# Kernel tuning notes

Measured on AMD Instinct MI355X. Metric: run time of the kernel, lower is better.

## Reference

```python
import jax, jax.numpy as jnp
import numpy as np

KS = 3  # deformable kernel size

def conv2d(x, w, pad, stride=1):
    return jax.lax.conv_general_dilated(
        x, w, (stride, stride), [(pad, pad), (pad, pad)],
        dimension_numbers=('NCHW', 'OIHW', 'NCHW'))

def deform_conv(x, wp, bp, wc):
    # Faithful port of DeformConv2d(inc, outc, kernel_size=3, padding=1, stride=1)
    b, c, h, w = x.shape
    N = KS * KS
    offset = conv2d(x, wp, 1) + bp[None, :, None, None]  # [b, 2N, h, w]
    xpad = jnp.pad(x, ((0, 0), (0, 0), (1, 1), (1, 1)))
    Hp, Wp = h + 2, w + 2
    # p_n: kernel-relative offsets (x coords first, then y coords)
    rng = jnp.arange(-(KS - 1) // 2, (KS - 1) // 2 + 1, dtype=x.dtype)
    pnx, pny = jnp.meshgrid(rng, rng, indexing='ij')
    p_n = jnp.concatenate([pnx.reshape(-1), pny.reshape(-1)])  # [2N]
    # p_0: base sampling grid (1-indexed into padded map)
    p0x = jnp.broadcast_to(jnp.arange(1, h + 1, dtype=x.dtype)[:, None], (h, w))
    p0y = jnp.broadcast_to(jnp.arange(1, w + 1, dtype=x.dtype)[None, :], (h, w))
    p0 = jnp.concatenate([jnp.broadcast_to(p0x, (N, h, w)),
                          jnp.broadcast_to(p0y, (N, h, w))], 0)  # [2N,h,w]
    p = p0[None] + p_n[None, :, None, None] + offset  # [b,2N,h,w]
    p = jnp.transpose(p, (0, 2, 3, 1))  # [b,h,w,2N]
    qf = jax.lax.stop_gradient(jnp.floor(p))
    qltx = jnp.clip(qf[..., :N], 0, Hp - 1)
    qlty = jnp.clip(qf[..., N:], 0, Wp - 1)
    qrbx = jnp.clip(qf[..., :N] + 1, 0, Hp - 1)
    qrby = jnp.clip(qf[..., N:] + 1, 0, Wp - 1)
    px = jnp.clip(p[..., :N], 0, Hp - 1)
    py = jnp.clip(p[..., N:], 0, Wp - 1)
    g_lt = (1 + (qltx - px)) * (1 + (qlty - py))
    g_rb = (1 - (qrbx - px)) * (1 - (qrby - py))
    g_lb = (1 + (qltx - px)) * (1 - (qrby - py))
    g_rt = (1 - (qrbx - px)) * (1 + (qlty - py))
    xflat = xpad.reshape(b, c, Hp * Wp)
    def gather(qx, qy):
        idx = (qx.astype(jnp.int32) * Wp + qy.astype(jnp.int32)).reshape(b, 1, -1)
        idx = jnp.broadcast_to(idx, (b, c, idx.shape[-1]))
        return jnp.take_along_axis(xflat, idx, axis=2).reshape(b, c, h, w, N)
    xo = (g_lt[:, None] * gather(qltx, qlty) + g_rb[:, None] * gather(qrbx, qrby)
          + g_lb[:, None] * gather(qltx, qrby) + g_rt[:, None] * gather(qrbx, qlty))
    # rearrange 'b c h w (i j) -> b c (h i) (w j)'
    xo = xo.reshape(b, c, h, w, KS, KS).transpose(0, 1, 2, 4, 3, 5).reshape(b, c, h * KS, w * KS)
    return conv2d(xo, wc, 1, stride=KS)


def setup_inputs() -> dict:
    key = jax.random.key(0)
    B, C, H, W = 4, 64, 256, 256
    DIM, S0 = 64, 5
    ks = jax.random.split(key, 14)
    s = 0.02
    inp = {
        'x': jax.random.normal(ks[0], (B, C, H, W), jnp.float32),
        'wp_a': jax.random.normal(ks[1], (2 * KS * KS, C, 3, 3), jnp.float32) * s,
        'bp_a': jnp.zeros((2 * KS * KS,), jnp.float32),
        'wc_a': jax.random.normal(ks[2], (C, C, KS, KS), jnp.float32) * s,
        'w1_a': jax.random.normal(ks[3], (C, C, 1, 1), jnp.float32) * s,
        'b1_a': jax.random.normal(ks[4], (C,), jnp.float32) * s,
        'wp_p': jax.random.normal(ks[5], (2 * KS * KS, C, 3, 3), jnp.float32) * s,
        'bp_p': jnp.zeros((2 * KS * KS,), jnp.float32),
        'wc_p': jax.random.normal(ks[6], (C, C, KS, KS), jnp.float32) * s,
        'w1_p': jax.random.normal(ks[7], (C, C, 1, 1), jnp.float32) * s,
        'b1_p': jax.random.normal(ks[8], (C,), jnp.float32) * s,
        'w0': jax.random.normal(ks[9], (DIM, C, S0, S0), jnp.float32) * s,
        'b0': jax.random.normal(ks[10], (DIM,), jnp.float32) * s,
    }
    return inp


def reference(x, wp_a, bp_a, wc_a, w1_a, b1_a, wp_p, bp_p, wc_p, w1_p, b1_p, w0, b0):
    H, W = x.shape[2], x.shape[3]
    xf = jnp.fft.rfft2(x, axes=(2, 3))
    amp = jnp.abs(xf)
    pha = jnp.angle(xf)
    amp3 = deform_conv(amp, wp_a, bp_a, wc_a)
    amp1 = conv2d(amp, w1_a, 0) + b1_a[None, :, None, None]
    pha3 = deform_conv(pha, wp_p, bp_p, wc_p)
    pha1 = conv2d(pha, w1_p, 0) + b1_p[None, :, None, None]
    eps = 1e-08
    real_13 = amp1 * jnp.cos(pha3) + eps
    imag_31 = amp3 * jnp.sin(pha1) + eps
    real_31 = amp3 * jnp.cos(pha1) + eps
    imag_13 = amp1 * jnp.sin(pha3) + eps
    out_c = (real_13 + real_31) + 1j * (imag_31 + imag_13) + eps
    xr = jnp.abs(jnp.fft.irfft2(out_c, s=(H, W), axes=(2, 3)))
    s0 = w0.shape[2]
    return conv2d(xr, w0, s0 // 2) + b0[None, :, None, None]
```

## Files before the change

kernel.cpp:

```cpp
#include <hip/hip_runtime.h>
#include <math.h>

#define BB 4
#define CC 64
#define HH 256
#define WW 256
#define WF 129
#define NPIX (WF*HH)
#define NS ((size_t)BB*CC*NPIX)
#define TWOPI 6.283185307179586f

typedef __attribute__((ext_vector_type(8))) short short8v;
typedef __attribute__((ext_vector_type(4))) float float4v;

__device__ __forceinline__ float2 cmulf(float2 a, float2 b) {
    return make_float2(a.x*b.x - a.y*b.y, a.x*b.y + a.y*b.x);
}

template<int SIGN>
__device__ __forceinline__ float2 fft256_lds(const float2* __restrict__ xs,
                                             float2* __restrict__ ys,
                                             const float2* __restrict__ tw,
                                             const float2* __restrict__ tw16,
                                             int t) {
    int k1 = t & 15, n2 = t >> 4;
    float2 acc = make_float2(0.f, 0.f);
    #pragma unroll
    for (int n1 = 0; n1 < 16; ++n1) {
        float2 v = xs[n1*16 + n2];
        float2 w = tw16[(n1*k1) & 15];
        float ws = (SIGN < 0) ? -w.y : w.y;
        acc.x = fmaf(v.x, w.x, fmaf(-v.y, ws, acc.x));
        acc.y = fmaf(v.x, ws, fmaf( v.y, w.x, acc.y));
    }
    float2 w2 = tw[n2*k1];
    float w2s = (SIGN < 0) ? -w2.y : w2.y;
    ys[t] = cmulf(acc, make_float2(w2.x, w2s));
    __syncthreads();
    float2 acc2 = make_float2(0.f, 0.f);
    #pragma unroll
    for (int m2 = 0; m2 < 16; ++m2) {
        float2 v = ys[m2*16 + k1];
        float2 w = tw16[(m2*n2) & 15];
        float ws = (SIGN < 0) ? -w.y : w.y;
        acc2.x = fmaf(v.x, w.x, fmaf(-v.y, ws, acc2.x));
        acc2.y = fmaf(v.x, ws, fmaf( v.y, w.x, acc2.y));
    }
    return acc2;
}

template<int SIGN>
__device__ __forceinline__ float2 fft256_ip(float2* __restrict__ buf,
                                            const float2* __restrict__ tw,
                                            const float2* __restrict__ tw16,
                                            int t) {
    int k1 = t & 15, n2 = t >> 4;
    float2 acc = make_float2(0.f, 0.f);
    #pragma unroll
    for (int n1 = 0; n1 < 16; ++n1) {
        float2 v = buf[n1*16 + n2];
        float2 w = tw16[(n1*k1) & 15];
        float ws = (SIGN < 0) ? -w.y : w.y;
        acc.x = fmaf(v.x, w.x, fmaf(-v.y, ws, acc.x));
        acc.y = fmaf(v.x, ws, fmaf( v.y, w.x, acc.y));
    }
    float2 w2 = tw[n2*k1];
    float w2s = (SIGN < 0) ? -w2.y : w2.y;
    float2 mid = cmulf(acc, make_float2(w2.x, w2s));
    __syncthreads();
    buf[t] = mid;
    __syncthreads();
    float2 acc2 = make_float2(0.f, 0.f);
    #pragma unroll
    for (int m2 = 0; m2 < 16; ++m2) {
        float2 v = buf[m2*16 + k1];
        float2 w = tw16[(m2*n2) & 15];
        float ws = (SIGN < 0) ? -w.y : w.y;
        acc2.x = fmaf(v.x, w.x, fmaf(-v.y, ws, acc2.x));
        acc2.y = fmaf(v.x, ws, fmaf( v.y, w.x, acc2.y));
    }
    return acc2;
}

__global__ void k_tw(float2* __restrict__ twg) {
    int m = threadIdx.x;
    float s, c;
    sincosf((TWOPI/256.f) * (float)m, &s, &c);
    twg[m] = make_float2(c, s);
}

__global__ __launch_bounds__(256) void k_fft_rows(const float* __restrict__ x,
                                                  const float2* __restrict__ twg,
                                                  float* __restrict__ r1re,
                                                  float* __restrict__ r1im) {
    __shared__ float2 work[256];
    __shared__ float tileRe[16][132], tileIm[16][132];
    __shared__ float2 tw[256];
    __shared__ float2 tw16[16];
    int t = threadIdx.x;
    int bid = blockIdx.x;
    int yt = bid & 15;
    int bc = bid >> 4;
    int y0 = yt*16;
    tw[t] = twg[t];
    if (t < 16) tw16[t] = twg[t*16];
    const float* xb = x + (size_t)bc*HH*WW + (size_t)y0*WW;
    for (int r = 0; r < 16; ++r) {
        __syncthreads();
        work[t] = make_float2(xb[r*WW + t], 0.f);
        __syncthreads();
        float2 X = fft256_ip<-1>(work, tw, tw16, t);
        if (t < WF) { tileRe[r][t] = X.x; tileIm[r][t] = X.y; }
    }
    __syncthreads();
    if (t < WF) {
        size_t base = ((size_t)bc*WF + t)*HH + y0;
        #pragma unroll
        for (int g = 0; g < 4; ++g) {
            float4 vr = make_float4(tileRe[g*4][t], tileRe[g*4+1][t],
                                    tileRe[g*4+2][t], tileRe[g*4+3][t]);
            float4 vi = make_float4(tileIm[g*4][t], tileIm[g*4+1][t],
                                    tileIm[g*4+2][t], tileIm[g*4+3][t]);
            *(float4*)&r1re[base + g*4] = vr;
            *(float4*)&r1im[base + g*4] = vi;
        }
    }
}

__global__ __launch_bounds__(256) void k_fft_cols(const float* __restrict__ r1re,
                                                  const float* __restrict__ r1im,
                                                  const float2* __restrict__ twg,
                                                  float* __restrict__ amp,
                                                  float* __restrict__ pha) {
    __shared__ float2 xs[256], ys[256];
    __shared__ float2 tw[256];
    __shared__ float2 tw16[16];
    int t = threadIdx.x;
    int bid = blockIdx.x;
    int k = bid % WF;
    int bc = bid / WF;
    size_t base = ((size_t)bc*WF + k)*HH;
    tw[t] = twg[t];
    if (t < 16) tw16[t] = twg[t*16];
    xs[t] = make_float2(r1re[base + t], r1im[base + t]);
    __syncthreads();
    float2 X = fft256_lds<-1>(xs, ys, tw, tw16, t);
    amp[base + t] = sqrtf(X.x*X.x + X.y*X.y);
    pha[base + t] = atan2f(X.y, X.x);
}

__global__ __launch_bounds__(256) void k_pack(const float* __restrict__ src,
                                              float* __restrict__ dst) {
    __shared__ float tile[64][65];
    int tid = threadIdx.x;
    int bid = blockIdx.x;
    int it = bid & 3;
    int rest = bid >> 2;
    int k = rest % WF;
    int b = rest / WF;
    int i0 = it*64;
    int ii = tid & 63;
    int cg = tid >> 6;
    for (int rep = 0; rep < 16; ++rep) {
        int c = cg*16 + rep;
        tile[c][ii] = src[(size_t)(b*CC + c)*NPIX + (size_t)k*HH + i0 + ii];
    }
    __syncthreads();
    for (int rep = 0; rep < 16; ++rep) {
        int m = cg*16 + rep;
        dst[((size_t)(b*WF + k)*HH + i0 + m)*CC + ii] = tile[ii][m];
    }
}

__device__ __forceinline__ unsigned short bf16r(float f) {
    unsigned u = __float_as_uint(f);
    unsigned r = (u + 0x7FFFu + ((u >> 16) & 1u)) >> 16;
    return (unsigned short)r;
}
__device__ __forceinline__ float bf16f(unsigned short h) {
    return __uint_as_float(((unsigned)h) << 16);
}

__global__ void k_wct(const float* __restrict__ wc,
                      unsigned short* __restrict__ wh,
                      unsigned short* __restrict__ wl) {
    int idx = blockIdx.x*256 + threadIdx.x;
    if (idx < 64*576) {
        int k = idx % 576;
        int oc = idx / 576;
        int pos = k >> 6;
        int c = k & 63;
        float v = wc[((size_t)oc*64 + c)*9 + pos];
        unsigned short h = bf16r(v);
        wh[idx] = h;
        wl[idx] = bf16r(v - bf16f(h));
    }
}

__global__ void k_wsplit(const float* __restrict__ w0,
                         unsigned short* __restrict__ whT,
                         unsigned short* __restrict__ wlT) {
    int idx = blockIdx.x*256 + threadIdx.x;
    if (idx < 25*64*64) {
        int c = idx & 63;
        int t = idx >> 6;
        int oc = t & 63;
        int tap = t >> 6;
        float v = w0[((size_t)oc*CC + c)*25 + tap];
        unsigned short h = bf16r(v);
        float l = v - bf16f(h);
        whT[idx] = h;
        wlT[idx] = bf16r(l);
    }
}

__global__ void k_wpt(const float* __restrict__ wpa, const float* __restrict__ wpp,
                      float* __restrict__ wta, float* __restrict__ wtp) {
    int idx = blockIdx.x*256 + threadIdx.x;
    if (idx < 64*162) {
        int c = idx / 162;
        int r = idx - c*162;
        int oc = r / 9, pos = r - oc*9;
        size_t s = ((size_t)oc*CC + c)*9 + pos;
        wta[idx] = wpa[s];
        wtp[idx] = wpp[s];
    }
}

__global__ __launch_bounds__(256) void k_off2(const float* __restrict__ amp,
                                              const float* __restrict__ pha,
                                              const float* __restrict__ wptA,
                                              const float* __restrict__ wptP,
                                              const float* __restrict__ bpA,
                                              const float* __restrict__ bpP,
                                              float* __restrict__ offa,
                                              float* __restrict__ offp) {
    __shared__ float colb[2][3][260];
    int tid = threadIdx.x;
    int bid = blockIdx.x;
    int sel = (bid >= BB*WF) ? 1 : 0;
    int rb = sel ? bid - BB*WF : bid;
    int j = rb % WF;
    int b = rb / WF;
    const float* img = sel ? pha : amp;
    const float* wpt = sel ? wptP : wptA;
    const float* bp  = sel ? bpP  : bpA;
    float* off = sel ? offp : offa;

    const float* ib = img + (size_t)b*CC*NPIX + (size_t)j*HH;
    bool jm = (j > 0), jp = (j < WF-1);

    float acc[18];
    #pragma unroll
    for (int o = 0; o < 18; ++o) acc[o] = bp[o];

    if (tid < 12) {
        int bufi = tid & 1;
        int dj = (tid >> 1) % 3;
        int e = tid / 6;
        colb[bufi][dj][e ? 257 : 0] = 0.f;
    }
    {
        const float* cb = ib;
        colb[0][1][tid+1] = cb[tid];
        colb[0][0][tid+1] = jm ? cb[tid - HH] : 0.f;
        colb[0][2][tid+1] = jp ? cb[tid + HH] : 0.f;
    }
    __syncthreads();

    for (int c = 0; c < CC; ++c) {
        int cur = c & 1;
        if (c + 1 < CC) {
            const float* cb = ib + (size_t)(c+1)*NPIX;
            colb[cur^1][1][tid+1] = cb[tid];
            colb[cur^1][0][tid+1] = jm ? cb[tid - HH] : 0.f;
            colb[cur^1][2][tid+1] = jp ? cb[tid + HH] : 0.f;
        }
        float v[9];
        #pragma unroll
        for (int di = 0; di < 3; ++di)
            #pragma unroll
            for (int dj = 0; dj < 3; ++dj)
                v[di*3+dj] = colb[cur][dj][tid + di];
        const float* wc = wpt + c*162;
        #pragma unroll
        for (int o = 0; o < 18; ++o) {
            #pragma unroll
            for (int p = 0; p < 9; ++p)
                acc[o] = fmaf(wc[o*9+p], v[p], acc[o]);
        }
        __syncthreads();
    }

    size_t ob = ((size_t)(b*18)*WF + j)*HH + tid;
    #pragma unroll
    for (int o = 0; o < 18; ++o)
        off[ob + (size_t)o*WF*HH] = acc[o];
}

#define SPAD 328
__global__ __launch_bounds__(256) void k_deform(const float* __restrict__ imgc,
                                                const float* __restrict__ off,
                                                const unsigned short* __restrict__ wh,
                                                const unsigned short* __restrict__ wl,
                                                float* __restrict__ out) {
    __shared__ int   cidx[4][144];
    __shared__ float cwgt[4][144];
    __shared__ __align__(16) unsigned short Sh[16][SPAD];
    __shared__ __align__(16) unsigned short Sl[16][SPAD];
    int tid = threadIdx.x;
    int bid = blockIdx.x;
    int it = bid & 15;
    int rest = bid >> 4;
    int j = rest % WF;
    int b = rest / WF;
    int i0 = it * 16;

    if (tid < 144) {
        int pix = tid / 9;
        int pos = tid % 9;
        int ki = pos / 3, kj = pos % 3;
        int i = i0 + pix;
        int r = 3*i + ki - 1;
        int s = 3*j + kj - 1;
        float g[4] = {0.f,0.f,0.f,0.f};
        int ix[4] = {-1,-1,-1,-1};
        if (r >= 0 && s >= 0) {
            int hq = r/3, nx = r%3;
            int wq = s/3, ny = s%3;
            int n = nx*3 + ny;
            float ox = off[((size_t)(b*18 + n)*WF + wq)*HH + hq];
            float oy = off[((size_t)(b*18 + 9 + n)*WF + wq)*HH + hq];
            float pxf = (float)(hq + nx) + ox;
            float pyf = (float)(wq + ny) + oy;
            float qx = floorf(pxf), qy = floorf(pyf);
            float qltx = fminf(fmaxf(qx, 0.f), 257.f);
            float qlty = fminf(fmaxf(qy, 0.f), 130.f);
            float qrbx = fminf(fmaxf(qx + 1.f, 0.f), 257.f);
            float qrby = fminf(fmaxf(qy + 1.f, 0.f), 130.f);
            float pxc = fminf(fmaxf(pxf, 0.f), 257.f);
            float pyc = fminf(fmaxf(pyf, 0.f), 130.f);
            float glt = (1.f + (qltx - pxc)) * (1.f + (qlty - pyc));
            float grb = (1.f - (qrbx - pxc)) * (1.f - (qrby - pyc));
            float glb = (1.f + (qltx - pxc)) * (1.f - (qrby - pyc));
            float grt = (1.f - (qrbx - pxc)) * (1.f + (qlty - pyc));
            int ax0 = (int)qltx, ax1 = (int)qrbx;
            int ay0 = (int)qlty, ay1 = (int)qrby;
            int cx[4] = {ax0, ax1, ax0, ax1};
            int cy[4] = {ay0, ay1, ay1, ay0};
            g[0]=glt; g[1]=grb; g[2]=glb; g[3]=grt;
            #pragma unroll
            for (int q = 0; q < 4; ++q) {
                int a = cx[q], bq = cy[q];
                ix[q] = (a >= 1 && a <= 256 && bq >= 1 && bq <= 129)
                        ? ((bq-1)*HH + (a-1))*CC : -1;
            }
        }
        #pragma unroll
        for (int q = 0; q < 4; ++q) { cidx[q][tid] = ix[q]; cwgt[q][tid] = g[q]; }
    }
    __syncthreads();

    const float* cb = imgc + (size_t)b * (size_t)WF * HH * CC;
    int lane = tid & 63;
    int w = tid >> 6;
    int l15 = lane & 15;
    int l4 = lane >> 4;
    float4v acc = {0.f, 0.f, 0.f, 0.f};
    const unsigned short* wbh = wh + (size_t)(w*16 + l15)*576 + l4*8;
    const unsigned short* wbl = wl + (size_t)(w*16 + l15)*576 + l4*8;

    for (int t = tid; t < 4096; t += 256) {
        int c = t & 63;
        int s = t >> 6;
        int pix = s >> 2, pos = s & 3;
        int combo = pix*9 + pos;
        float sum = 0.f;
        #pragma unroll
        for (int q = 0; q < 4; ++q) {
            int ofs = cidx[q][combo];
            float v = (ofs >= 0) ? cb[(size_t)ofs + c] : 0.f;
            sum += cwgt[q][combo] * v;
        }
        unsigned short h = bf16r(sum);
        Sh[pix][pos*64 + c] = h;
        Sl[pix][pos*64 + c] = bf16r(sum - bf16f(h));
    }
    __syncthreads();
    #pragma unroll
    for (int k0 = 0; k0 < 256; k0 += 32) {
        short8v Ah = *(const short8v*)&wbh[k0];
        short8v Al = *(const short8v*)&wbl[k0];
        short8v Bh = *(const short8v*)&Sh[l15][k0 + l4*8];
        short8v Bl = *(const short8v*)&Sl[l15][k0 + l4*8];
        acc = __builtin_amdgcn_mfma_f32_16x16x32_bf16(Ah, Bh, acc, 0, 0, 0);
        acc = __builtin_amdgcn_mfma_f32_16x16x32_bf16(Ah, Bl, acc, 0, 0, 0);
        acc = __builtin_amdgcn_mfma_f32_16x16x32_bf16(Al, Bh, acc, 0, 0, 0);
    }
    __syncthreads();

    for (int t = tid; t < 5120; t += 256) {
        int c = t & 63;
        int s = t >> 6;
        int pix = s / 5, pp = s - pix*5;
        int combo = pix*9 + 4 + pp;
        float sum = 0.f;
        #pragma unroll
        for (int q = 0; q < 4; ++q) {
            int ofs = cidx[q][combo];
            float v = (ofs >= 0) ? cb[(size_t)ofs + c] : 0.f;
            sum += cwgt[q][combo] * v;
        }
        unsigned short h = bf16r(sum);
        Sh[pix][pp*64 + c] = h;
        Sl[pix][pp*64 + c] = bf16r(sum - bf16f(h));
    }
    __syncthreads();
    #pragma unroll
    for (int k0 = 0; k0 < 320; k0 += 32) {
        short8v Ah = *(const short8v*)&wbh[256 + k0];
        short8v Al = *(const short8v*)&wbl[256 + k0];
        short8v Bh = *(const short8v*)&Sh[l15][k0 + l4*8];
        short8v Bl = *(const short8v*)&Sl[l15][k0 + l4*8];
        acc = __builtin_amdgcn_mfma_f32_16x16x32_bf16(Ah, Bh, acc, 0, 0, 0);
        acc = __builtin_amdgcn_mfma_f32_16x16x32_bf16(Ah, Bl, acc, 0, 0, 0);
        acc = __builtin_amdgcn_mfma_f32_16x16x32_bf16(Al, Bh, acc, 0, 0, 0);
    }

    size_t ob = (size_t)b*CC*NPIX + (size_t)j*HH + i0;
    #pragma unroll
    for (int r = 0; r < 4; ++r) {
        int oc = w*16 + l4*4 + r;
        out[ob + (size_t)oc*NPIX + l15] = acc[r];
    }
}

__global__ __launch_bounds__(256) void k_combine(const float* __restrict__ ampc,
                                                 const float* __restrict__ phac,
                                                 float* __restrict__ a3,
                                                 float* __restrict__ p3,
                                                 const float* __restrict__ w1a,
                                                 const float* __restrict__ b1a,
                                                 const float* __restrict__ w1p,
                                                 const float* __restrict__ b1p) {
    __shared__ float la[64][65], lp[64][65];
    int tid = threadIdx.x;
    int bid = blockIdx.x;
    int quarter = bid & 3;
    int rest = bid >> 2;
    int j = rest % WF;
    int b = rest / WF;
    int i0 = quarter * 64;
    size_t gbase = ((size_t)(b*WF + j)*HH + i0) * CC;
    for (int rep = 0; rep < 16; ++rep) {
        int t = rep*256 + tid;
        int pix = t >> 6;
        int c = t & 63;
        la[c][pix] = ampc[gbase + t];
        lp[c][pix] = phac[gbase + t];
    }
    __syncthreads();
    int ii = tid & 63;
    int wv = tid >> 6;
    float acc_a[16], acc_p[16];
    #pragma unroll
    for (int q = 0; q < 16; ++q) { acc_a[q] = b1a[wv*16+q]; acc_p[q] = b1p[wv*16+q]; }
    for (int c = 0; c < CC; ++c) {
        float av = la[c][ii], pv = lp[c][ii];
        #pragma unroll
        for (int q = 0; q < 16; ++q) {
            acc_a[q] += w1a[(wv*16+q)*CC + c] * av;
            acc_p[q] += w1p[(wv*16+q)*CC + c] * pv;
        }
    }
    #pragma unroll
    for (int q = 0; q < 16; ++q) {
        int oc = wv*16 + q;
        size_t idx = (size_t)(b*CC + oc)*NPIX + (size_t)j*HH + i0 + ii;
        float a3v = a3[idx];
        float p3v = p3[idx];
        float s1, c1, s3, c3;
        sincosf(acc_p[q], &s1, &c1);
        sincosf(p3v, &s3, &c3);
        float re = acc_a[q]*c3 + a3v*c1 + 3e-8f;
        float im = a3v*s1 + acc_a[q]*s3 + 2e-8f;
        a3[idx] = re;
        p3[idx] = im;
    }
}

__global__ __launch_bounds__(256) void k_ifft_cols(const float* __restrict__ ocre,
                                                   const float* __restrict__ ocim,
                                                   const float2* __restrict__ twg,
                                                   float* __restrict__ r2re,
                                                   float* __restrict__ r2im) {
    __shared__ float2 xs[256], ys[256];
    __shared__ float2 tw[256];
    __shared__ float2 tw16[16];
    int t = threadIdx.x;
    int bid = blockIdx.x;
    int k = bid % WF;
    int bc = bid / WF;
    size_t base = ((size_t)bc*WF + k)*HH;
    tw[t] = twg[t];
    if (t < 16) tw16[t] = twg[t*16];
    xs[t] = make_float2(ocre[base + t], ocim[base + t]);
    __syncthreads();
    float2 X = fft256_lds<1>(xs, ys, tw, tw16, t);
    r2re[base + t] = X.x * (1.0f/256.0f);
    r2im[base + t] = X.y * (1.0f/256.0f);
}

__global__ __launch_bounds__(256) void k_irfft_rows(const float* __restrict__ r2re,
                                                    const float* __restrict__ r2im,
                                                    const float2* __restrict__ twg,
                                                    float* __restrict__ xr) {
    __shared__ float2 work[256];
    __shared__ float tileRe[16][132], tileIm[16][132];
    __shared__ float2 tw[256];
    __shared__ float2 tw16[16];
    int t = threadIdx.x;
    int bid = blockIdx.x;
    int yt = bid & 15;
    int bc = bid >> 4;
    int y0 = yt*16;
    tw[t] = twg[t];
    if (t < 16) tw16[t] = twg[t*16];
    if (t < WF) {
        size_t base = ((size_t)bc*WF + t)*HH + y0;
        #pragma unroll
        for (int g = 0; g < 4; ++g) {
            float4 vr = *(const float4*)&r2re[base + g*4];
            float4 vi = *(const float4*)&r2im[base + g*4];
            tileRe[g*4+0][t] = vr.x; tileIm[g*4+0][t] = vi.x;
            tileRe[g*4+1][t] = vr.y; tileIm[g*4+1][t] = vi.y;
            tileRe[g*4+2][t] = vr.z; tileIm[g*4+2][t] = vi.z;
            tileRe[g*4+3][t] = vr.w; tileIm[g*4+3][t] = vi.w;
        }
    }
    __syncthreads();
    float* xb = xr + (size_t)bc*HH*WW + (size_t)y0*WW;
    int src = (t < WF) ? t : 256 - t;
    float sg = (t < WF) ? 1.f : -1.f;
    for (int r = 0; r < 16; ++r) {
        work[t] = make_float2(tileRe[r][src], sg*tileIm[r][src]);
        __syncthreads();
        float2 X = fft256_ip<1>(work, tw, tw16, t);
        xb[r*WW + t] = fabsf(X.x * (1.0f/256.0f));
        __syncthreads();
    }
}

__global__ __launch_bounds__(256) void k_split(const float* __restrict__ xr,
                                               unsigned short* __restrict__ xh,
                                               unsigned short* __restrict__ xl) {
    __shared__ float tile[64][65];
    int tid = threadIdx.x;
    int bid = blockIdx.x;
    int q = bid & 3;
    int y = (bid >> 2) & 255;
    int b = bid >> 10;
    int x0 = q*64;
    int lane = tid & 63;
    int cg = tid >> 6;
    for (int rep = 0; rep < 16; ++rep) {
        int c = cg*16 + rep;
        tile[c][lane] = xr[(((size_t)(b*CC + c)*HH + y)*WW) + x0 + lane];
    }
    __syncthreads();
    int x = tid >> 2;
    int c0 = (tid & 3)*8;
    #pragma unroll
    for (int ch = 0; ch < 2; ++ch) {
        short8v hv, lv;
        #pragma unroll
        for (int j = 0; j < 8; ++j) {
            float v = tile[ch*32 + c0 + j][x];
            unsigned short h = bf16r(v);
            float l = v - bf16f(h);
            hv[j] = (short)h;
            lv[j] = (short)bf16r(l);
        }
        size_t ob = ((((size_t)(b*2 + ch)*HH + y)*WW) + x0 + x)*32 + c0;
        *(short8v*)&xh[ob] = hv;
        *(short8v*)&xl[ob] = lv;
    }
}

#define LROW 40
#define LX 72
#define LROWS 6
#define PLANE (LROWS*LX*LROW)
#define NSLOT 7

__global__ __launch_bounds__(256) void k_conv5m(const unsigned short* __restrict__ xh,
                                                const unsigned short* __restrict__ xl,
                                                const unsigned short* __restrict__ whT,
                                                const unsigned short* __restrict__ wlT,
                                                const float* __restrict__ b0,
                                                float* __restrict__ out) {
    __shared__ unsigned short smem[2*PLANE];
    int tid = threadIdx.x;
    int bid = blockIdx.x;
    int q = bid & 3;
    int yb = (bid >> 2) & 127;
    int b = bid >> 9;
    int x0 = q*64;
    int y0 = yb*2;
    int lane = tid & 63;
    int w = tid >> 6;
    int wrow = w >> 1;
    int oc0 = (w & 1)*32;
    int l15 = lane & 15;
    int l4  = lane >> 4;

    int goff[NSLOT], loff[NSLOT];
    bool inb[NSLOT], okimg[NSLOT];
    #pragma unroll
    for (int s = 0; s < NSLOT; ++s) {
        int it = tid + s*256;
        int part = it & 3;
        int idx = it >> 2;
        int row = idx / LX;
        int xi = idx - row*LX;
        int gy = y0 + row - 2;
        int gx = x0 + xi - 2;
        bool ib = (it < LROWS*LX*4);
        bool ok = ib && gy >= 0 && gy < HH && gx >= 0 && gx < WW;
        inb[s] = ib;
        okimg[s] = ok;
        goff[s] = ok ? ((gy*WW + gx)*32 + part*8) : 0;
        loff[s] = ib ? ((row*LX + xi)*LROW + part*8) : 0;
    }

    float4v acc[2][4];
    #pragma unroll
    for (int o = 0; o < 2; ++o) {
        float4v bi;
        #pragma unroll
        for (int r = 0; r < 4; ++r) bi[r] = b0[oc0 + o*16 + l4*4 + r];
        #pragma unroll
        for (int p = 0; p < 4; ++p) acc[o][p] = bi;
    }

    short8v rh[NSLOT], rl[NSLOT];
    const short8v zero8 = {0,0,0,0,0,0,0,0};

#define PREFETCH(CH) do { \
        size_t chb = ((size_t)(b*2 + (CH)) << 16) * 32; \
        _Pragma("unroll") \
        for (int s = 0; s < NSLOT; ++s) { \
            rh[s] = *(const short8v*)&xh[chb + goff[s]]; \
            rl[s] = *(const short8v*)&xl[chb + goff[s]]; \
        } \
    } while (0)

#define WRITE() do { \
        _Pragma("unroll") \
        for (int s = 0; s < NSLOT; ++s) { \
            if (inb[s]) { \
                *(short8v*)&smem[loff[s]]         = okimg[s] ? rh[s] : zero8; \
                *(short8v*)&smem[PLANE + loff[s]] = okimg[s] ? rl[s] : zero8; \
            } \
        } \
    } while (0)

#define LOADA(TAP, CH, A0, A1, A2, A3r) do { \
        size_t wb = ((size_t)(TAP)*64 + oc0 + l15)*64 + (size_t)(CH)*32 + l4*8; \
        A0  = *(const short8v*)&whT[wb]; \
        A1  = *(const short8v*)&whT[wb + 1024]; \
        A2  = *(const short8v*)&wlT[wb]; \
        A3r = *(const short8v*)&wlT[wb + 1024]; \
    } while (0)

#define LOADB(TAP, B_h, B_l) do { \
        int dy = (TAP)/5, dx = (TAP) - dy*5; \
        int rbase = (wrow + dy)*LX + l15 + dx; \
        _Pragma("unroll") \
        for (int p = 0; p < 4; ++p) { \
            int a = (rbase + p*16)*LROW + l4*8; \
            B_h[p] = *(const short8v*)&smem[a]; \
            B_l[p] = *(const short8v*)&smem[a + PLANE]; \
        } \
    } while (0)

#define MFMAS(A0, A1, A2, A3r, B_h, B_l) do { \
        _Pragma("unroll") for (int p = 0; p < 4; ++p) \
            acc[0][p] = __builtin_amdgcn_mfma_f32_16x16x32_bf16(A0, B_h[p], acc[0][p], 0, 0, 0); \
        _Pragma("unroll") for (int p = 0; p < 4; ++p) \
            acc[1][p] = __builtin_amdgcn_mfma_f32_16x16x32_bf16(A1, B_h[p], acc[1][p], 0, 0, 0); \
        _Pragma("unroll") for (int p = 0; p < 4; ++p) \
            acc[0][p] = __builtin_amdgcn_mfma_f32_16x16x32_bf16(A0, B_l[p], acc[0][p], 0, 0, 0); \
        _Pragma("unroll") for (int p = 0; p < 4; ++p) \
            acc[1][p] = __builtin_amdgcn_mfma_f32_16x16x32_bf16(A1, B_l[p], acc[1][p], 0, 0, 0); \
        _Pragma("unroll") for (int p = 0; p < 4; ++p) \
            acc[0][p] = __builtin_amdgcn_mfma_f32_16x16x32_bf16(A2, B_h[p], acc[0][p], 0, 0, 0); \
        _Pragma("unroll") for (int p = 0; p < 4; ++p) \
            acc[1][p] = __builtin_amdgcn_mfma_f32_16x16x32_bf16(A3r, B_h[p], acc[1][p], 0, 0, 0); \
    } while (0)

#define COMPUTE(CH) do { \
        short8v cA0, cA1, cA2, cA3, nA0, nA1, nA2, nA3; \
        short8v cBh[4], cBl[4]; \
        LOADA(0, CH, cA0, cA1, cA2, cA3); \
        _Pragma("unroll 5") \
        for (int tap = 0; tap < 25; ++tap) { \
            if (tap < 24) LOADA(tap+1, CH, nA0, nA1, nA2, nA3); \
            LOADB(tap, cBh, cBl); \
            MFMAS(cA0, cA1, cA2, cA3, cBh, cBl); \
            if (tap < 24) { cA0 = nA0; cA1 = nA1; cA2 = nA2; cA3 = nA3; } \
        } \
    } while (0)

    PREFETCH(0);
    WRITE();
    __syncthreads();
    PREFETCH(1);
    COMPUTE(0);
    __syncthreads();
    WRITE();
    __syncthreads();
    COMPUTE(1);

#undef PREFETCH
#undef WRITE
#undef LOADA
#undef LOADB
#undef MFMAS
#undef COMPUTE

    int y = y0 + wrow;
    #pragma unroll
    for (int o = 0; o < 2; ++o) {
        #pragma unroll
        for (int p = 0; p < 4; ++p) {
            #pragma unroll
            for (int r = 0; r < 4; ++r) {
                int oc = oc0 + o*16 + l4*4 + r;
                int x = x0 + p*16 + l15;
                out[(((size_t)(b*CC + oc)*HH + y)*WW) + x] = acc[o][p][r];
            }
        }
    }
}

extern "C" void kernel_launch(void* const* d_in, const int* in_sizes, int n_in,
                              void* d_out, int out_size, void* d_ws, size_t ws_size,
                              hipStream_t stream) {
    const float* x    = (const float*)d_in[0];
    const float* wp_a = (const float*)d_in[1];
    const float* bp_a = (const float*)d_in[2];
    const float* wc_a = (const float*)d_in[3];
    const float* w1_a = (const float*)d_in[4];
    const float* b1_a = (const float*)d_in[5];
    const float* wp_p = (const float*)d_in[6];
    const float* bp_p = (const float*)d_in[7];
    const float* wc_p = (const float*)d_in[8];
    const float* w1_p = (const float*)d_in[9];
    const float* b1_p = (const float*)d_in[10];
    const float* w0   = (const float*)d_in[11];
    const float* b0   = (const float*)d_in[12];
    float* out = (float*)d_out;
    float* ws  = (float*)d_ws;

    float* R0 = ws;
    float* R1 = ws + 2*NS;
    float* R2 = ws + 4*NS;

    float* r1re = R0;
    float* r1im = R0 + NS;
    float* amp  = R1;
    float* pha  = R1 + NS;
    float* ampc = R0;
    float* phac = R0 + NS;
    size_t offsz = (size_t)BB*18*NPIX;
    float* offa = R2;
    float* offp = R2 + offsz;
    unsigned short* wsp = (unsigned short*)(R2 + 2*offsz);
    unsigned short* whA = wsp;
    unsigned short* wlA = wsp + 36864;
    unsigned short* whP = wsp + 2*36864;
    unsigned short* wlP = wsp + 3*36864;
    unsigned short* whT = wsp + 4*36864;
    unsigned short* wlT = whT + 25*64*64;
    float* wptA = (float*)(wlT + 25*64*64);
    float* wptP = wptA + 64*162;
    float2* twg = (float2*)(wptP + 64*162);
    float* A3   = R1;
    float* P3   = R1 + NS;
    float* r2re = R0;
    float* r2im = R0 + NS;
    float* xrp  = R1;
    unsigned short* xhp = (unsigned short*)R0;
    unsigned short* xlp = xhp + (size_t)BB*2*HH*WW*32;

    k_tw<<<1, 256, 0, stream>>>(twg);
    k_wct<<<144, 256, 0, stream>>>(wc_a, whA, wlA);
    k_wct<<<144, 256, 0, stream>>>(wc_p, whP, wlP);
    k_wsplit<<<400, 256, 0, stream>>>(w0, whT, wlT);
    k_wpt<<<41, 256, 0, stream>>>(wp_a, wp_p, wptA, wptP);
    k_fft_rows<<<BB*CC*16, 256, 0, stream>>>(x, twg, r1re, r1im);
    k_fft_cols<<<BB*CC*WF, 256, 0, stream>>>(r1re, r1im, twg, amp, pha);
    k_pack<<<BB*WF*4, 256, 0, stream>>>(amp, ampc);
    k_pack<<<BB*WF*4, 256, 0, stream>>>(pha, phac);
    k_off2<<<2*BB*WF, 256, 0, stream>>>(amp, pha, wptA, wptP, bp_a, bp_p, offa, offp);
    k_deform<<<BB*WF*16, 256, 0, stream>>>(ampc, offa, whA, wlA, A3);
    k_deform<<<BB*WF*16, 256, 0, stream>>>(phac, offp, whP, wlP, P3);
    k_combine<<<BB*WF*4, 256, 0, stream>>>(ampc, phac, A3, P3, w1_a, b1_a, w1_p, b1_p);
    k_ifft_cols<<<BB*CC*WF, 256, 0, stream>>>(A3, P3, twg, r2re, r2im);
    k_irfft_rows<<<BB*CC*16, 256, 0, stream>>>(r2re, r2im, twg, xrp);
    k_split<<<BB*HH*4, 256, 0, stream>>>(xrp, xhp, xlp);
    k_conv5m<<<BB*128*4, 256, 0, stream>>>(xhp, xlp, whT, wlT, b0, out);
}
```

Measured before the change: 1.454 ms.

## Rework final 5x5 conv to 32x32x16 MFMA with 4-row tiles

The final 5x5 convolution kernel moves from 16x16x32 bf16 MFMAs to 32x32x16 MFMAs. Each block now covers 4 output rows (one per wave) and all 64 output channels, so the grid is halved. The input channel dimension is staged through LDS in four 16-channel phases with register prefetch, which shrinks the LDS tile and adds more syncs. The aim is fewer LDS B-operand reads per MFMA flop and better weight reuse, at the cost of dropping the A-operand prefetch and adding sync points.

```diff
diff --git a/kernel.cpp b/kernel.cpp
--- a/kernel.cpp
+++ b/kernel.cpp
@@ -12,6 +12,7 @@
 
 typedef __attribute__((ext_vector_type(8))) short short8v;
 typedef __attribute__((ext_vector_type(4))) float float4v;
+typedef __attribute__((ext_vector_type(16))) float float16v;
 
 __device__ __forceinline__ float2 cmulf(float2 a, float2 b) {
     return make_float2(a.x*b.x - a.y*b.y, a.x*b.y + a.y*b.x);
@@ -587,11 +588,9 @@
     }
 }
 
-#define LROW 40
-#define LX 72
-#define LROWS 6
-#define PLANE (LROWS*LX*LROW)
-#define NSLOT 7
+#define CLX 68
+#define CPART 544
+#define CPLANE 1088
 
 __global__ __launch_bounds__(256) void k_conv5m(const unsigned short* __restrict__ xh,
                                                 const unsigned short* __restrict__ xl,
@@ -599,116 +598,99 @@
                                                 const unsigned short* __restrict__ wlT,
                                                 const float* __restrict__ b0,
                                                 float* __restrict__ out) {
-    __shared__ unsigned short smem[2*PLANE];
+    __shared__ __align__(16) unsigned short smem[2*CPLANE*8];
     int tid = threadIdx.x;
     int bid = blockIdx.x;
     int q = bid & 3;
-    int yb = (bid >> 2) & 127;
-    int b = bid >> 9;
+    int yb = (bid >> 2) & 63;
+    int b = bid >> 8;
     int x0 = q*64;
-    int y0 = yb*2;
+    int y0 = yb*4;
     int lane = tid & 63;
     int w = tid >> 6;
-    int wrow = w >> 1;
-    int oc0 = (w & 1)*32;
-    int l15 = lane & 15;
-    int l4  = lane >> 4;
-
-    int goff[NSLOT], loff[NSLOT];
-    bool inb[NSLOT], okimg[NSLOT];
-    #pragma unroll
-    for (int s = 0; s < NSLOT; ++s) {
-        int it = tid + s*256;
-        int part = it & 3;
-        int idx = it >> 2;
-        int row = idx / LX;
-        int xi = idx - row*LX;
+    int l31 = lane & 31;
+    int l1  = lane >> 5;
+
+    int goffb[5], loffs[5];
+    bool ok[5], has[5];
+    #pragma unroll
+    for (int s = 0; s < 5; ++s) {
+        int item = (s < 4) ? (s*256 + tid) : (1024 + tid);
+        bool h = (s < 4) || (tid < 64);
+        int part = (item >= CPART) ? 1 : 0;
+        int rest = item - part*CPART;
+        int row = rest / CLX;
+        int xi = rest - row*CLX;
         int gy = y0 + row - 2;
         int gx = x0 + xi - 2;
-        bool ib = (it < LROWS*LX*4);
-        bool ok = ib && gy >= 0 && gy < HH && gx >= 0 && gx < WW;
-        inb[s] = ib;
-        okimg[s] = ok;
-        goff[s] = ok ? ((gy*WW + gx)*32 + part*8) : 0;
-        loff[s] = ib ? ((row*LX + xi)*LROW + part*8) : 0;
-    }
-
-    float4v acc[2][4];
-    #pragma unroll
-    for (int o = 0; o < 2; ++o) {
-        float4v bi;
-        #pragma unroll
-        for (int r = 0; r < 4; ++r) bi[r] = b0[oc0 + o*16 + l4*4 + r];
-        #pragma unroll
-        for (int p = 0; p < 4; ++p) acc[o][p] = bi;
-    }
-
-    short8v rh[NSLOT], rl[NSLOT];
+        bool o = h && gy >= 0 && gy < HH && gx >= 0 && gx < WW;
+        has[s] = h; ok[s] = o;
+        goffb[s] = o ? ((gy*WW + gx)*32 + part*8) : 0;
+        loffs[s] = (part*CPART + row*CLX + xi)*8;
+    }
+
+    float16v acc[2][2];
+    #pragma unroll
+    for (int o2 = 0; o2 < 2; ++o2) {
+        float16v bi;
+        #pragma unroll
+        for (int r = 0; r < 16; ++r)
+            bi[r] = b0[o2*32 + (r & 3) + 8*(r >> 2) + 4*l1];
+        acc[o2][0] = bi;
+        acc[o2][1] = bi;
+    }
+
+    short8v rh[5], rl[5];
     const short8v zero8 = {0,0,0,0,0,0,0,0};
 
-#define PREFETCH(CH) do { \
-        size_t chb = ((size_t)(b*2 + (CH)) << 16) * 32; \
+#define PREFETCH(P) do { \
+        size_t chb = ((size_t)(b*2 + ((P) >> 1)) << 16) * 32; \
+        int phofs = ((P) & 1) * 16; \
         _Pragma("unroll") \
-        for (int s = 0; s < NSLOT; ++s) { \
-            rh[s] = *(const short8v*)&xh[chb + goff[s]]; \
-            rl[s] = *(const short8v*)&xl[chb + goff[s]]; \
-        } \
-    } while (0)
-
-#define WRITE() do { \
-        _Pragma("unroll") \
-        for (int s = 0; s < NSLOT; ++s) { \
-            if (inb[s]) { \
-                *(short8v*)&smem[loff[s]]         = okimg[s] ? rh[s] : zero8; \
-                *(short8v*)&smem[PLANE + loff[s]] = okimg[s] ? rl[s] : zero8; \
+        for (int s = 0; s < 5; ++s) { \
+            if (has[s]) { \
+                rh[s] = *(const short8v*)&xh[chb + goffb[s] + phofs]; \
+                rl[s] = *(const short8v*)&xl[chb + goffb[s] + phofs]; \
             } \
         } \
     } while (0)
 
-#define LOADA(TAP, CH, A0, A1, A2, A3r) do { \
-        size_t wb = ((size_t)(TAP)*64 + oc0 + l15)*64 + (size_t)(CH)*32 + l4*8; \
-        A0  = *(const short8v*)&whT[wb]; \
-        A1  = *(const short8v*)&whT[wb + 1024]; \
-        A2  = *(const short8v*)&wlT[wb]; \
-        A3r = *(const short8v*)&wlT[wb + 1024]; \
-    } while (0)
-
-#define LOADB(TAP, B_h, B_l) do { \
-        int dy = (TAP)/5, dx = (TAP) - dy*5; \
-        int rbase = (wrow + dy)*LX + l15 + dx; \
+#define WRITE() do { \
         _Pragma("unroll") \
-        for (int p = 0; p < 4; ++p) { \
-            int a = (rbase + p*16)*LROW + l4*8; \
-            B_h[p] = *(const short8v*)&smem[a]; \
-            B_l[p] = *(const short8v*)&smem[a + PLANE]; \
+        for (int s = 0; s < 5; ++s) { \
+            if (has[s]) { \
+                *(short8v*)&smem[loffs[s]]              = ok[s] ? rh[s] : zero8; \
+                *(short8v*)&smem[CPLANE*8 + loffs[s]]   = ok[s] ? rl[s] : zero8; \
+            } \
         } \
     } while (0)
 
-#define MFMAS(A0, A1, A2, A3r, B_h, B_l) do { \
-        _Pragma("unroll") for (int p = 0; p < 4; ++p) \
-            acc[0][p] = __builtin_amdgcn_mfma_f32_16x16x32_bf16(A0, B_h[p], acc[0][p], 0, 0, 0); \
-        _Pragma("unroll") for (int p = 0; p < 4; ++p) \
-            acc[1][p] = __builtin_amdgcn_mfma_f32_16x16x32_bf16(A1, B_h[p], acc[1][p], 0, 0, 0); \
-        _Pragma("unroll") for (int p = 0; p < 4; ++p) \
-            acc[0][p] = __builtin_amdgcn_mfma_f32_16x16x32_bf16(A0, B_l[p], acc[0][p], 0, 0, 0); \
-        _Pragma("unroll") for (int p = 0; p < 4; ++p) \
-            acc[1][p] = __builtin_amdgcn_mfma_f32_16x16x32_bf16(A1, B_l[p], acc[1][p], 0, 0, 0); \
-        _Pragma("unroll") for (int p = 0; p < 4; ++p) \
-            acc[0][p] = __builtin_amdgcn_mfma_f32_16x16x32_bf16(A2, B_h[p], acc[0][p], 0, 0, 0); \
-        _Pragma("unroll") for (int p = 0; p < 4; ++p) \
-            acc[1][p] = __builtin_amdgcn_mfma_f32_16x16x32_bf16(A3r, B_h[p], acc[1][p], 0, 0, 0); \
-    } while (0)
-
-#define COMPUTE(CH) do { \
-        short8v cA0, cA1, cA2, cA3, nA0, nA1, nA2, nA3; \
-        short8v cBh[4], cBl[4]; \
-        LOADA(0, CH, cA0, cA1, cA2, cA3); \
+#define COMPUTE(P) do { \
         _Pragma("unroll 5") \
         for (int tap = 0; tap < 25; ++tap) { \
-            if (tap < 24) LOADA(tap+1, CH, nA0, nA1, nA2, nA3); \
-            LOADB(tap, cBh, cBl); \
-            MFMAS(cA0, cA1, cA2, cA3, cBh, cBl); \
-            if (tap < 24) { cA0 = nA0; cA1 = nA1; cA2 = nA2; cA3 = nA3; } \
+            int dy = tap / 5, dx = tap - dy*5; \
+            size_t wb = ((size_t)(tap*64 + l31))*64 + (P)*16 + l1*8; \
+            short8v Ah0 = *(const short8v*)&whT[wb]; \
+            short8v Al0 = *(const short8v*)&wlT[wb]; \
+            short8v Ah1 = *(const short8v*)&whT[wb + 2048]; \
+            short8v Al1 = *(const short8v*)&wlT[wb + 2048]; \
+            int a0 = (l1*CPART + (w + dy)*CLX + l31 + dx)*8; \
+            short8v Bh0 = *(const short8v*)&smem[a0]; \
+            short8v Bl0 = *(const short8v*)&smem[CPLANE*8 + a0]; \
+            short8v Bh1 = *(const short8v*)&smem[a0 + 256]; \
+            short8v Bl1 = *(const short8v*)&smem[CPLANE*8 + a0 + 256]; \
+            acc[0][0] = __builtin_amdgcn_mfma_f32_32x32x16_bf16(Ah0, Bh0, acc[0][0], 0,0,0); \
+            acc[0][1] = __builtin_amdgcn_mfma_f32_32x32x16_bf16(Ah0, Bh1, acc[0][1], 0,0,0); \
+            acc[1][0] = __builtin_amdgcn_mfma_f32_32x32x16_bf16(Ah1, Bh0, acc[1][0], 0,0,0); \
+            acc[1][1] = __builtin_amdgcn_mfma_f32_32x32x16_bf16(Ah1, Bh1, acc[1][1], 0,0,0); \
+            acc[0][0] = __builtin_amdgcn_mfma_f32_32x32x16_bf16(Ah0, Bl0, acc[0][0], 0,0,0); \
+            acc[0][1] = __builtin_amdgcn_mfma_f32_32x32x16_bf16(Ah0, Bl1, acc[0][1], 0,0,0); \
+            acc[1][0] = __builtin_amdgcn_mfma_f32_32x32x16_bf16(Ah1, Bl0, acc[1][0], 0,0,0); \
+            acc[1][1] = __builtin_amdgcn_mfma_f32_32x32x16_bf16(Ah1, Bl1, acc[1][1], 0,0,0); \
+            acc[0][0] = __builtin_amdgcn_mfma_f32_32x32x16_bf16(Al0, Bh0, acc[0][0], 0,0,0); \
+            acc[0][1] = __builtin_amdgcn_mfma_f32_32x32x16_bf16(Al0, Bh1, acc[0][1], 0,0,0); \
+            acc[1][0] = __builtin_amdgcn_mfma_f32_32x32x16_bf16(Al1, Bh0, acc[1][0], 0,0,0); \
+            acc[1][1] = __builtin_amdgcn_mfma_f32_32x32x16_bf16(Al1, Bh1, acc[1][1], 0,0,0); \
         } \
     } while (0)
 
@@ -720,25 +702,32 @@
     __syncthreads();
     WRITE();
     __syncthreads();
+    PREFETCH(2);
     COMPUTE(1);
+    __syncthreads();
+    WRITE();
+    __syncthreads();
+    PREFETCH(3);
+    COMPUTE(2);
+    __syncthreads();
+    WRITE();
+    __syncthreads();
+    COMPUTE(3);
 
 #undef PREFETCH
 #undef WRITE
-#undef LOADA
-#undef LOADB
-#undef MFMAS
 #undef COMPUTE
 
-    int y = y0 + wrow;
-    #pragma unroll
-    for (int o = 0; o < 2; ++o) {
-        #pragma unroll
-        for (int p = 0; p < 4; ++p) {
+    int y = y0 + w;
+    #pragma unroll
+    for (int o2 = 0; o2 < 2; ++o2) {
+        #pragma unroll
+        for (int p2 = 0; p2 < 2; ++p2) {
             #pragma unroll
-            for (int r = 0; r < 4; ++r) {
-                int oc = oc0 + o*16 + l4*4 + r;
-                int x = x0 + p*16 + l15;
-                out[(((size_t)(b*CC + oc)*HH + y)*WW) + x] = acc[o][p][r];
+            for (int r = 0; r < 16; ++r) {
+                int oc = o2*32 + (r & 3) + 8*(r >> 2) + 4*l1;
+                int x = x0 + p2*32 + l31;
+                out[(((size_t)(b*CC + oc)*HH + y)*WW) + x] = acc[o2][p2][r];
             }
         }
     }
@@ -810,5 +799,5 @@
     k_ifft_cols<<<BB*CC*WF, 256, 0, stream>>>(A3, P3, twg, r2re, r2im);
     k_irfft_rows<<<BB*CC*16, 256, 0, stream>>>(r2re, r2im, twg, xrp);
     k_split<<<BB*HH*4, 256, 0, stream>>>(xrp, xhp, xlp);
-    k_conv5m<<<BB*128*4, 256, 0, stream>>>(xhp, xlp, whT, wlT, b0, out);
-}
+    k_conv5m<<<BB*64*4, 256, 0, stream>>>(xhp, xlp, whT, wlT, b0, out);
+}
```

Result: no change. 1.464 ms (+0.7%).
